# Optimization experiments

Measured on AMD Instinct MI355X. Metric: run time of the kernel, lower is better.

Reference implementation:

```python
import jax, jax.numpy as jnp
import numpy as np

KS = 3          # deformable kernel size
N = KS * KS     # 9 sampling points
PAD = 1         # zero padding before sampling


def setup_inputs() -> dict:
    key = jax.random.key(0)
    k = jax.random.split(key, 4)
    b, c, h, w = 8, 64, 128, 128
    x = jax.random.normal(k[0], (b, c, h, w), jnp.float32)
    # offset-prediction conv: Conv2d(c, 2*N, 3, padding=1, stride=1) with bias
    w_off = jax.random.normal(k[1], (2 * N, c, 3, 3), jnp.float32) * 0.01
    b_off = jax.random.normal(k[2], (2 * N,), jnp.float32) * 0.01
    # main conv: Conv2d(c, c, 3, stride=3, bias=None) applied to rearranged samples
    w_conv = jax.random.normal(k[3], (c, c, KS, KS), jnp.float32) * (1.0 / np.sqrt(c * N))
    return {"x": x, "w_off": w_off, "b_off": b_off, "w_conv": w_conv}


def _deform_conv2d(x, w_off, b_off, w_conv):
    b, c, h, w = x.shape
    # 1) predict offsets: (b, 2N, h, w)
    offset = jax.lax.conv_general_dilated(
        x, w_off, (1, 1), ((PAD, PAD), (PAD, PAD)),
        dimension_numbers=("NCHW", "OIHW", "NCHW"))
    offset = offset + b_off[None, :, None, None]
    offset = offset.transpose(0, 2, 3, 1)  # (b, h, w, 2N), first N = rows, last N = cols

    # 2) sampling positions p = p_0 + p_n + offset (in zero-padded coords)
    dx, dy = jnp.meshgrid(
        jnp.arange(-(KS - 1) // 2, (KS - 1) // 2 + 1),
        jnp.arange(-(KS - 1) // 2, (KS - 1) // 2 + 1), indexing="ij")
    pn_x = dx.reshape(-1).astype(x.dtype)  # (N,)
    pn_y = dy.reshape(-1).astype(x.dtype)
    r0 = jnp.arange(1, h + 1, dtype=x.dtype)  # p_0 starts at 1 (padding shift)
    c0 = jnp.arange(1, w + 1, dtype=x.dtype)
    p_x = offset[..., :N] + pn_x + r0[None, :, None, None]   # (b,h,w,N)
    p_y = offset[..., N:] + pn_y + c0[None, None, :, None]

    xp = jnp.pad(x, ((0, 0), (0, 0), (PAD, PAD), (PAD, PAD)))
    Hp, Wp = h + 2 * PAD, w + 2 * PAD

    fx = jnp.floor(p_x)
    fy = jnp.floor(p_y)
    q_lt_x = jnp.clip(fx, 0, Hp - 1).astype(jnp.int32)
    q_lt_y = jnp.clip(fy, 0, Wp - 1).astype(jnp.int32)
    q_rb_x = jnp.clip(fx + 1, 0, Hp - 1).astype(jnp.int32)
    q_rb_y = jnp.clip(fy + 1, 0, Wp - 1).astype(jnp.int32)
    p_x = jnp.clip(p_x, 0, Hp - 1)
    p_y = jnp.clip(p_y, 0, Wp - 1)

    # bilinear weights (b,h,w,N); q values are non-differentiable (int)
    g_lt = (1 + (q_lt_x - p_x)) * (1 + (q_lt_y - p_y))
    g_rb = (1 - (q_rb_x - p_x)) * (1 - (q_rb_y - p_y))
    g_lb = (1 + (q_lt_x - p_x)) * (1 - (q_rb_y - p_y))
    g_rt = (1 - (q_rb_x - p_x)) * (1 + (q_lt_y - p_y))

    xp_flat = xp.reshape(b, c, Hp * Wp)

    def gather(qx, qy):
        idx = (qx * Wp + qy).reshape(b, 1, h * w * N)
        out = jnp.take_along_axis(
            xp_flat, jnp.broadcast_to(idx, (b, c, h * w * N)), axis=2)
        return out.reshape(b, c, h, w, N)

    x_off = (g_lt[:, None] * gather(q_lt_x, q_lt_y)
             + g_rb[:, None] * gather(q_rb_x, q_rb_y)
             + g_lb[:, None] * gather(q_lt_x, q_rb_y)
             + g_rt[:, None] * gather(q_rb_x, q_lt_y))  # (b,c,h,w,N)

    # 3) final KSxKS conv with stride KS over the rearranged samples is exactly
    #    a contraction over the N sampling points (sample n = kernel tap (i,j), n=i*KS+j)
    out = jnp.einsum("bchwn,ocn->bohw", x_off, w_conv.reshape(c, c, N))
    return out


def reference(x, w_off, b_off, w_conv):
    return _deform_conv2d(x, w_off, b_off, w_conv) + x
```

## Files before the change

kernel.cpp:

```cpp
#include <hip/hip_runtime.h>


typedef _Float16 h2    __attribute__((ext_vector_type(2)));
typedef _Float16 f16x8 __attribute__((ext_vector_type(8)));
typedef float    f32x4 __attribute__((ext_vector_type(4)));

#define MFMAH(a, b, c) __builtin_amdgcn_mfma_f32_16x16x32_f16(a, b, c, 0, 0, 0)

__device__ __forceinline__ unsigned short f2h(float f) {
    return __builtin_bit_cast(unsigned short, (_Float16)f);
}
__device__ __forceinline__ float h2f_bits(unsigned u) {
    return (float)__builtin_bit_cast(_Float16, (unsigned short)(u & 0xffffu));
}
__device__ __forceinline__ unsigned dup16(float g) {
    _Float16 t = (_Float16)g;
    h2 r = {t, t};
    return __builtin_bit_cast(unsigned, r);
}

__global__ __launch_bounds__(256) void k_prep_xt(const float* __restrict__ x,
                                                 unsigned short* __restrict__ xt) {
    __shared__ float xs[64][129];
    const int bh = blockIdx.x;
    const int h = bh & 127, b = bh >> 7;
    const float* xr = x + ((size_t)b * 64 * 128 + h) * 128;
    for (int idx = threadIdx.x; idx < 8192; idx += 256) {
        int c = idx >> 7, w = idx & 127;
        xs[c][w] = xr[(size_t)c * 16384 + w];
    }
    __syncthreads();
    unsigned short* xto = xt + ((size_t)bh << 13);
    for (int j = threadIdx.x; j < 1024; j += 256) {
        int w = j >> 3, c0 = (j & 7) << 3;
        unsigned short tmp[8];
#pragma unroll
        for (int e = 0; e < 8; ++e) tmp[e] = f2h(xs[c0 + e][w]);
        *(uint4*)(xto + w * 64 + c0) = *(const uint4*)tmp;
    }
}

__global__ void k_prep_w(const float* __restrict__ w_conv, const float* __restrict__ w_off,
                         unsigned short* __restrict__ w_m2, unsigned short* __restrict__ woff2) {
    int t = blockIdx.x * 256 + threadIdx.x;
    if (t < 36864) {
        int r = t & 511;
        int fid = t >> 9;
        int l15 = r >> 5, q4 = (r >> 3) & 3, e = t & 7;
        int chunk = fid & 1, of = (fid >> 1) & 3, n = fid >> 3;
        int o = of * 16 + l15, c = chunk * 32 + q4 * 8 + e;
        w_m2[t] = f2h(w_conv[(o * 64 + c) * 9 + n]);
    }
    int t2 = t - 36864;
    if (t2 >= 0 && t2 < 18432) {
        int r = t2 & 511;
        int fid = t2 >> 9;
        int l15 = r >> 5, q4 = (r >> 3) & 3, e = t2 & 7;
        int kc = fid & 1, half = (fid >> 1) & 1, rj = fid >> 2;
        int k = half * 16 + l15, c = kc * 32 + q4 * 8 + e;
        woff2[t2] = (k < 18) ? f2h(w_off[(k * 64 + c) * 9 + rj]) : (unsigned short)0;
    }
}

__global__ __launch_bounds__(256, 4) void k_fused(
    const float* __restrict__ x, const unsigned short* __restrict__ xt,
    const unsigned short* __restrict__ w_m2, const unsigned short* __restrict__ woff2,
    const float* __restrict__ b_off, float* __restrict__ out) {

    __shared__ __align__(16) unsigned char raw[4 * 70 * 128];
    __shared__ __align__(16) _Float16 offv[64 * 24];
    __shared__ int sfb;

    const int wk = ((blockIdx.x & 7) << 8) + (blockIdx.x >> 3);
    const int b = wk >> 8, h = (wk >> 1) & 127, wt = (wk & 1) << 6;

    const int tid  = threadIdx.x;
    const int lane = tid & 63, wid = tid >> 6;
    const int l15  = lane & 15, q4 = lane >> 4;
    const int lofs = ((l15 << 2) + q4) << 3;
    const int px   = wid * 16 + l15;

    const unsigned short* xtb = xt + ((size_t)b << 20);
    const _Float16* wmh  = (const _Float16*)w_m2;

    if (tid == 0) sfb = 0;

    for (int idx = tid; idx < 2240; idx += 256) {
        int rec = idx >> 3, cc = idx & 7;
        int rl = rec / 70, col = rec - rl * 70;
        int xr = h - 2 + rl, xc = wt - 3 + col;
        uint4 v = make_uint4(0, 0, 0, 0);
        if (xr >= 0 && xr < 128 && xc >= 0 && xc < 128)
            v = *(const uint4*)(xtb + ((((size_t)xr << 7) + xc) << 6) + (cc << 3));
        *(uint4*)(raw + (rec << 7) + ((cc ^ (col & 7)) << 4)) = v;
    }
    __syncthreads();

    {
        f32x4 o0 = {0.f, 0.f, 0.f, 0.f}, o1 = {0.f, 0.f, 0.f, 0.f};
#pragma unroll
        for (int rj = 0; rj < 9; ++rj) {
            const int dr = rj / 3, dj = rj % 3;
            const int colw = px + dj + 2;
            const int recb = (dr + 1) * 70 + colw;
            const int swz  = colw & 7;
#pragma unroll
            for (int kc = 0; kc < 2; ++kc) {
                f16x8 bfrag = *(const f16x8*)(raw + (recb << 7) + ((((kc << 2) + q4) ^ swz) << 4));
                f16x8 a0 = *(const f16x8*)((const _Float16*)woff2 + ((((rj * 2 + 0) << 1) + kc) << 9) + lofs);
                f16x8 a1 = *(const f16x8*)((const _Float16*)woff2 + ((((rj * 2 + 1) << 1) + kc) << 9) + lofs);
                o0 = MFMAH(a0, bfrag, o0);
                o1 = MFMAH(a1, bfrag, o1);
            }
        }
        float4 bo = *(const float4*)(b_off + (q4 << 2));
        float2 bo2 = *(const float2*)(b_off + 16);
        const float bov[4] = {bo.x, bo.y, bo.z, bo.w};
#pragma unroll
        for (int rg = 0; rg < 4; ++rg) {
            int o = (q4 << 2) + rg;
            offv[px * 24 + o] = (_Float16)(o0[rg] + bov[rg]);
            if (q4 == 0 && rg < 2) offv[px * 24 + 16 + rg] = (_Float16)(o1[rg] + (rg ? bo2.y : bo2.x));
        }
    }
    __syncthreads();

    for (int idx = tid; idx < 576; idx += 256) {
        const int n = idx >> 6, p = idx & 63;
        const int dr = n / 3, dj = n % 3;
        float ox = (float)offv[p * 24 + n], oy = (float)offv[p * 24 + 9 + n];
        float pxf = (float)(h + dr) + ox, pyf = (float)(wt + p + dj) + oy;
        float fx = floorf(pxf), fy = floorf(pyf);
        int qx0 = (int)fminf(fmaxf(fx, 0.f), 129.f);
        int qx1 = (int)fminf(fmaxf(fx + 1.f, 0.f), 129.f);
        int qy0 = (int)fminf(fmaxf(fy, 0.f), 129.f);
        int qy1 = (int)fminf(fmaxf(fy + 1.f, 0.f), 129.f);
        int r0 = qx0 - h - dr, r1 = qx1 - h - dr;
        int c0 = qy0 - wt + 2, c1 = qy1 - wt + 2;
        bool oow = (r0 < -1) | (r0 > 2) | (r1 < -1) | (r1 > 2) |
                   (c0 < 0) | (c0 >= 70) | (c1 < 0) | (c1 >= 70);
        if (oow) sfb = 1;
    }
    __syncthreads();
    const bool slow = (sfb != 0);

    f32x4 acc[4];
#pragma unroll
    for (int of = 0; of < 4; ++of) acc[of] = (f32x4){0.f, 0.f, 0.f, 0.f};

    auto blend = [&](const uint4* clo, const uint4* chi, uint4 gq, f16x8& bfr0, f16x8& bfr1) {
        h2 g0 = __builtin_bit_cast(h2, gq.x), g1 = __builtin_bit_cast(h2, gq.y);
        h2 g2 = __builtin_bit_cast(h2, gq.z), g3 = __builtin_bit_cast(h2, gq.w);
        const unsigned* c0 = (const unsigned*)&clo[0];
        const unsigned* c1 = (const unsigned*)&clo[1];
        const unsigned* c2 = (const unsigned*)&clo[2];
        const unsigned* c3 = (const unsigned*)&clo[3];
        const unsigned* e0 = (const unsigned*)&chi[0];
        const unsigned* e1 = (const unsigned*)&chi[1];
        const unsigned* e2 = (const unsigned*)&chi[2];
        const unsigned* e3 = (const unsigned*)&chi[3];
        unsigned owl[4], owh[4];
#pragma unroll
        for (int d = 0; d < 4; ++d) {
            h2 sl = __builtin_bit_cast(h2, c0[d]) * g0;
            sl = __builtin_elementwise_fma(__builtin_bit_cast(h2, c1[d]), g1, sl);
            sl = __builtin_elementwise_fma(__builtin_bit_cast(h2, c2[d]), g2, sl);
            sl = __builtin_elementwise_fma(__builtin_bit_cast(h2, c3[d]), g3, sl);
            owl[d] = __builtin_bit_cast(unsigned, sl);
            h2 sh = __builtin_bit_cast(h2, e0[d]) * g0;
            sh = __builtin_elementwise_fma(__builtin_bit_cast(h2, e1[d]), g1, sh);
            sh = __builtin_elementwise_fma(__builtin_bit_cast(h2, e2[d]), g2, sh);
            sh = __builtin_elementwise_fma(__builtin_bit_cast(h2, e3[d]), g3, sh);
            owh[d] = __builtin_bit_cast(unsigned, sh);
        }
        bfr0 = __builtin_bit_cast(f16x8, *(const uint4*)owl);
        bfr1 = __builtin_bit_cast(f16x8, *(const uint4*)owh);
    };

    if (!slow) {
        const unsigned* op = (const unsigned*)(offv + px * 24);
        uint4 oA = *(const uint4*)op;
        uint4 oB = *(const uint4*)(op + 4);
        unsigned oC = op[8];
        const unsigned ow[9] = {oA.x, oA.y, oA.z, oA.w, oB.x, oB.y, oB.z, oB.w, oC};
#define OX(n) h2f_bits(ow[(n) >> 1] >> (((n) & 1) << 4))
#define OY(n) h2f_bits(ow[(9 + (n)) >> 1] >> (((9 + (n)) & 1) << 4))

        uint4 pf[3];
        int pcol[3], pcc[3];
#pragma unroll
        for (int k = 0; k < 3; ++k) {
            int idx = tid + (k << 8);
            bool v = idx < 560;
            int rec = idx >> 3;
            pcol[k] = v ? rec : 0;
            pcc[k]  = idx & 7;
            int xr = h + 2, xc = wt - 3 + pcol[k];
            uint4 vv = make_uint4(0, 0, 0, 0);
            if (v && xr < 128 && xc >= 0 && xc < 128)
                vv = *(const uint4*)(xtb + ((((size_t)xr << 7) + xc) << 6) + (pcc[k] << 3));
            if (!v) pcol[k] = -1;
            pf[k] = vv;
        }

#define TAP(n)                                                                           \
        {                                                                                \
            constexpr int dr = (n) / 3, dj = (n) % 3;                                    \
            const _Float16* wn = wmh + ((n) << 12);                                      \
            f16x8 wa0[4], wa1[4];                                                        \
            _Pragma("unroll")                                                            \
            for (int of = 0; of < 4; ++of) {                                             \
                wa0[of] = *(const f16x8*)(wn + (((of << 1) + 0) << 9) + lofs);           \
                wa1[of] = *(const f16x8*)(wn + (((of << 1) + 1) << 9) + lofs);           \
            }                                                                            \
            float ox = OX(n), oy = OY(n);                                                \
            float pxf = (float)(h + dr) + ox, pyf = (float)(wt + px + dj) + oy;          \
            float fx = floorf(pxf), fy = floorf(pyf);                                    \
            float qx0f = fminf(fmaxf(fx, 0.f), 129.f);                                   \
            float qx1f = fminf(fmaxf(fx + 1.f, 0.f), 129.f);                             \
            float qy0f = fminf(fmaxf(fy, 0.f), 129.f);                                   \
            float qy1f = fminf(fmaxf(fy + 1.f, 0.f), 129.f);                             \
            float pxc = fminf(fmaxf(pxf, 0.f), 129.f);                                   \
            float pyc = fminf(fmaxf(pyf, 0.f), 129.f);                                   \
            float ax0 = 1.f + (qx0f - pxc), ax1 = 1.f - (qx1f - pxc);                    \
            float ay0 = 1.f + (qy0f - pyc), ay1 = 1.f - (qy1f - pyc);                    \
            int s0 = ((((int)qx0f + 1 - h) & 3) * 70) << 7;                              \
            int s1 = ((((int)qx1f + 1 - h) & 3) * 70) << 7;                              \
            int c0 = (int)qy0f - wt + 2, c1 = (int)qy1f - wt + 2;                        \
            int blt = s0 + (c0 << 7), brb = s1 + (c1 << 7);                              \
            int blb = s0 + (c1 << 7), brt = s1 + (c0 << 7);                              \
            int z0 = ((q4 ^ c0) & 7) << 4, z1 = ((q4 ^ c1) & 7) << 4;                    \
            uint4 clo[4], chi[4];                                                        \
            clo[0] = *(const uint4*)(raw + blt + z0); chi[0] = *(const uint4*)(raw + blt + (z0 ^ 64)); \
            clo[1] = *(const uint4*)(raw + brb + z1); chi[1] = *(const uint4*)(raw + brb + (z1 ^ 64)); \
            clo[2] = *(const uint4*)(raw + blb + z1); chi[2] = *(const uint4*)(raw + blb + (z1 ^ 64)); \
            clo[3] = *(const uint4*)(raw + brt + z0); chi[3] = *(const uint4*)(raw + brt + (z0 ^ 64)); \
            uint4 gq = make_uint4(dup16(ax0 * ay0), dup16(ax1 * ay1),                    \
                                  dup16(ax0 * ay1), dup16(ax1 * ay0));                   \
            f16x8 bfr0, bfr1;                                                            \
            blend(clo, chi, gq, bfr0, bfr1);                                             \
            _Pragma("unroll")                                                            \
            for (int of = 0; of < 4; ++of) {                                             \
                acc[of] = MFMAH(wa0[of], bfr0, acc[of]);                                 \
                acc[of] = MFMAH(wa1[of], bfr1, acc[of]);                                 \
            }                                                                            \
        }

        TAP(0) TAP(1) TAP(2)
        __syncthreads();
#pragma unroll
        for (int k = 0; k < 3; ++k)
            if (pcol[k] >= 0)
                *(uint4*)(raw + ((0 * 70 + pcol[k]) << 7) + ((pcc[k] ^ (pcol[k] & 7)) << 4)) = pf[k];
        __syncthreads();
#pragma unroll
        for (int k = 0; k < 3; ++k) {
            int idx = tid + (k << 8);
            bool v = idx < 560;
            int rec = idx >> 3;
            pcol[k] = v ? rec : -1;
            pcc[k]  = idx & 7;
            int xr = h + 3, xc = wt - 3 + rec;
            uint4 vv = make_uint4(0, 0, 0, 0);
            if (v && xr < 128 && xc >= 0 && xc < 128)
                vv = *(const uint4*)(xtb + ((((size_t)xr << 7) + xc) << 6) + (pcc[k] << 3));
            pf[k] = vv;
        }
        TAP(3) TAP(4) TAP(5)
        __syncthreads();
#pragma unroll
        for (int k = 0; k < 3; ++k)
            if (pcol[k] >= 0)
                *(uint4*)(raw + ((1 * 70 + pcol[k]) << 7) + ((pcc[k] ^ (pcol[k] & 7)) << 4)) = pf[k];
        __syncthreads();
        TAP(6) TAP(7) TAP(8)
#undef TAP
#undef OX
#undef OY
    } else {
        for (int n = 0; n < 9; ++n) {
            const int dr = n / 3, dj = n % 3;
            float ox = (float)offv[px * 24 + n], oy = (float)offv[px * 24 + 9 + n];
            float pxf = (float)(h + dr) + ox, pyf = (float)(wt + px + dj) + oy;
            float fx = floorf(pxf), fy = floorf(pyf);
            float qx0f = fminf(fmaxf(fx, 0.f), 129.f);
            float qx1f = fminf(fmaxf(fx + 1.f, 0.f), 129.f);
            float qy0f = fminf(fmaxf(fy, 0.f), 129.f);
            float qy1f = fminf(fmaxf(fy + 1.f, 0.f), 129.f);
            float pxc = fminf(fmaxf(pxf, 0.f), 129.f);
            float pyc = fminf(fmaxf(pyf, 0.f), 129.f);
            float ax0 = 1.f + (qx0f - pxc), ax1 = 1.f - (qx1f - pxc);
            float ay0 = 1.f + (qy0f - pyc), ay1 = 1.f - (qy1f - pyc);
            int qx[2] = {(int)qx0f, (int)qx1f};
            int qy[2] = {(int)qy0f, (int)qy1f};
            uint4 clo[4], chi[4];
            const int rsel[4] = {0, 1, 0, 1}, csel[4] = {0, 1, 1, 0};
#pragma unroll
            for (int j = 0; j < 4; ++j) {
                int rx = qx[rsel[j]], ry = qy[csel[j]];
                bool v = (rx >= 1) & (rx <= 128) & (ry >= 1) & (ry <= 128);
                clo[j] = make_uint4(0, 0, 0, 0);
                chi[j] = make_uint4(0, 0, 0, 0);
                if (v) {
                    const unsigned short* gp = xtb + ((((size_t)(rx - 1) << 7) + (ry - 1)) << 6);
                    clo[j] = *(const uint4*)(gp + (q4 << 3));
                    chi[j] = *(const uint4*)(gp + (q4 << 3) + 32);
                }
            }
            uint4 gq = make_uint4(dup16(ax0 * ay0), dup16(ax1 * ay1),
                                  dup16(ax0 * ay1), dup16(ax1 * ay0));
            f16x8 bfr0, bfr1;
            blend(clo, chi, gq, bfr0, bfr1);
            const _Float16* wn = wmh + (n << 12);
#pragma unroll
            for (int of = 0; of < 4; ++of) {
                f16x8 a0 = *(const f16x8*)(wn + (((of << 1) + 0) << 9) + lofs);
                f16x8 a1 = *(const f16x8*)(wn + (((of << 1) + 1) << 9) + lofs);
                acc[of] = MFMAH(a0, bfr0, acc[of]);
                acc[of] = MFMAH(a1, bfr1, acc[of]);
            }
        }
    }

    const size_t obase = ((size_t)b * 64 * 128 + h) * 128 + wt + px;
#pragma unroll
    for (int of = 0; of < 4; ++of)
#pragma unroll
        for (int rg = 0; rg < 4; ++rg) {
            size_t a = obase + (size_t)((of << 4) + (q4 << 2) + rg) * 16384;
            out[a] = acc[of][rg] + x[a];
        }
}

extern "C" void kernel_launch(void* const* d_in, const int* in_sizes, int n_in,
                              void* d_out, int out_size, void* d_ws, size_t ws_size,
                              hipStream_t stream) {
    const float* x      = (const float*)d_in[0];
    const float* w_off  = (const float*)d_in[1];
    const float* b_off  = (const float*)d_in[2];
    const float* w_conv = (const float*)d_in[3];

    unsigned short* xt    = (unsigned short*)d_ws;
    unsigned short* w_m2  = xt + (size_t)8 * 128 * 128 * 64;
    unsigned short* woff2 = w_m2 + 9 * 64 * 64;

    hipLaunchKernelGGL(k_prep_xt, dim3(1024), dim3(256), 0, stream, x, xt);
    hipLaunchKernelGGL(k_prep_w,  dim3(216),  dim3(256), 0, stream, w_conv, w_off, w_m2, woff2);
    hipLaunchKernelGGL(k_fused,   dim3(2048), dim3(256), 0, stream,
                       x, xt, w_m2, woff2, b_off, (float*)d_out);
}
```

Before: 84.55 us.

## Process two output rows per block to reuse weights and halo rows

Each fused block now computes two adjacent output rows instead of one, halving the grid. The shared halo grows from 4 to 5 rows, so the overlapping input rows are loaded once and shared by both rows. The main-conv weight fragments for each tap are loaded once and used for both rows' MFMAs. In exchange the kernel holds twice the accumulators and a larger LDS footprint, and its launch bounds drop from 4 to 3 waves, which lowers occupancy and may cause register pressure.

```diff
diff --git a/kernel.cpp b/kernel.cpp
--- a/kernel.cpp
+++ b/kernel.cpp
@@ -62,17 +62,17 @@
     }
 }
 
-__global__ __launch_bounds__(256, 4) void k_fused(
+__global__ __launch_bounds__(256, 3) void k_fused(
     const float* __restrict__ x, const unsigned short* __restrict__ xt,
     const unsigned short* __restrict__ w_m2, const unsigned short* __restrict__ woff2,
     const float* __restrict__ b_off, float* __restrict__ out) {
 
-    __shared__ __align__(16) unsigned char raw[4 * 70 * 128];
-    __shared__ __align__(16) _Float16 offv[64 * 24];
+    __shared__ __align__(16) unsigned char raw[5 * 70 * 128];
+    __shared__ __align__(16) _Float16 offv[2][64][24];
     __shared__ int sfb;
 
-    const int wk = ((blockIdx.x & 7) << 8) + (blockIdx.x >> 3);
-    const int b = wk >> 8, h = (wk >> 1) & 127, wt = (wk & 1) << 6;
+    const int wk = ((blockIdx.x & 7) << 7) | (blockIdx.x >> 3);
+    const int b = wk >> 7, h = ((wk >> 1) & 63) << 1, wt = (wk & 1) << 6;
 
     const int tid  = threadIdx.x;
     const int lane = tid & 63, wid = tid >> 6;
@@ -85,7 +85,7 @@
 
     if (tid == 0) sfb = 0;
 
-    for (int idx = tid; idx < 2240; idx += 256) {
+    for (int idx = tid; idx < 2800; idx += 256) {
         int rec = idx >> 3, cc = idx & 7;
         int rl = rec / 70, col = rec - rl * 70;
         int xr = h - 2 + rl, xc = wt - 3 + col;
@@ -96,13 +96,14 @@
     }
     __syncthreads();
 
-    {
+#pragma unroll
+    for (int rr = 0; rr < 2; ++rr) {
         f32x4 o0 = {0.f, 0.f, 0.f, 0.f}, o1 = {0.f, 0.f, 0.f, 0.f};
 #pragma unroll
         for (int rj = 0; rj < 9; ++rj) {
             const int dr = rj / 3, dj = rj % 3;
             const int colw = px + dj + 2;
-            const int recb = (dr + 1) * 70 + colw;
+            const int recb = (rr + dr + 1) * 70 + colw;
             const int swz  = colw & 7;
 #pragma unroll
             for (int kc = 0; kc < 2; ++kc) {
@@ -119,34 +120,40 @@
 #pragma unroll
         for (int rg = 0; rg < 4; ++rg) {
             int o = (q4 << 2) + rg;
-            offv[px * 24 + o] = (_Float16)(o0[rg] + bov[rg]);
-            if (q4 == 0 && rg < 2) offv[px * 24 + 16 + rg] = (_Float16)(o1[rg] + (rg ? bo2.y : bo2.x));
+            offv[rr][px][o] = (_Float16)(o0[rg] + bov[rg]);
+            if (q4 == 0 && rg < 2) offv[rr][px][16 + rg] = (_Float16)(o1[rg] + (rg ? bo2.y : bo2.x));
         }
     }
     __syncthreads();
 
-    for (int idx = tid; idx < 576; idx += 256) {
-        const int n = idx >> 6, p = idx & 63;
-        const int dr = n / 3, dj = n % 3;
-        float ox = (float)offv[p * 24 + n], oy = (float)offv[p * 24 + 9 + n];
-        float pxf = (float)(h + dr) + ox, pyf = (float)(wt + p + dj) + oy;
+    for (int idx = tid; idx < 1152; idx += 256) {
+        const int p = idx & 63;
+        int rest = idx >> 6;
+        const int rr = (rest >= 9) ? 1 : 0;
+        const int n = rest - rr * 9;
+        const int g = n / 3, dj = n % 3;
+        float ox = (float)offv[rr][p][n], oy = (float)offv[rr][p][9 + n];
+        float pxf = (float)(h + rr + g) + ox, pyf = (float)(wt + p + dj) + oy;
         float fx = floorf(pxf), fy = floorf(pyf);
         int qx0 = (int)fminf(fmaxf(fx, 0.f), 129.f);
         int qx1 = (int)fminf(fmaxf(fx + 1.f, 0.f), 129.f);
         int qy0 = (int)fminf(fmaxf(fy, 0.f), 129.f);
         int qy1 = (int)fminf(fmaxf(fy + 1.f, 0.f), 129.f);
-        int r0 = qx0 - h - dr, r1 = qx1 - h - dr;
+        int t0 = qx0 + 1 - h - g, t1 = qx1 + 1 - h - g;
         int c0 = qy0 - wt + 2, c1 = qy1 - wt + 2;
-        bool oow = (r0 < -1) | (r0 > 2) | (r1 < -1) | (r1 > 2) |
-                   (c0 < 0) | (c0 >= 70) | (c1 < 0) | (c1 >= 70);
+        bool oow = ((unsigned)t0 > 4u) | ((unsigned)t1 > 4u) |
+                   ((unsigned)c0 > 69u) | ((unsigned)c1 > 69u);
         if (oow) sfb = 1;
     }
     __syncthreads();
     const bool slow = (sfb != 0);
 
-    f32x4 acc[4];
-#pragma unroll
-    for (int of = 0; of < 4; ++of) acc[of] = (f32x4){0.f, 0.f, 0.f, 0.f};
+    f32x4 acc0[4], acc1[4];
+#pragma unroll
+    for (int of = 0; of < 4; ++of) {
+        acc0[of] = (f32x4){0.f, 0.f, 0.f, 0.f};
+        acc1[of] = (f32x4){0.f, 0.f, 0.f, 0.f};
+    }
 
     auto blend = [&](const uint4* clo, const uint4* chi, uint4 gq, f16x8& bfr0, f16x8& bfr1) {
         h2 g0 = __builtin_bit_cast(h2, gq.x), g1 = __builtin_bit_cast(h2, gq.y);
@@ -178,13 +185,16 @@
     };
 
     if (!slow) {
-        const unsigned* op = (const unsigned*)(offv + px * 24);
-        uint4 oA = *(const uint4*)op;
-        uint4 oB = *(const uint4*)(op + 4);
-        unsigned oC = op[8];
-        const unsigned ow[9] = {oA.x, oA.y, oA.z, oA.w, oB.x, oB.y, oB.z, oB.w, oC};
-#define OX(n) h2f_bits(ow[(n) >> 1] >> (((n) & 1) << 4))
-#define OY(n) h2f_bits(ow[(9 + (n)) >> 1] >> (((9 + (n)) & 1) << 4))
+        const unsigned* op0 = (const unsigned*)&offv[0][px][0];
+        const unsigned* op1 = (const unsigned*)&offv[1][px][0];
+        uint4 oA0 = *(const uint4*)op0, oB0 = *(const uint4*)(op0 + 4);
+        unsigned oC0 = op0[8];
+        uint4 oA1 = *(const uint4*)op1, oB1 = *(const uint4*)(op1 + 4);
+        unsigned oC1 = op1[8];
+        const unsigned ow0[9] = {oA0.x, oA0.y, oA0.z, oA0.w, oB0.x, oB0.y, oB0.z, oB0.w, oC0};
+        const unsigned ow1[9] = {oA1.x, oA1.y, oA1.z, oA1.w, oB1.x, oB1.y, oB1.z, oB1.w, oC1};
+#define OXQ(arr, n) h2f_bits(arr[(n) >> 1] >> (((n) & 1) << 4))
+#define OYQ(arr, n) h2f_bits(arr[(9 + (n)) >> 1] >> (((9 + (n)) & 1) << 4))
 
         uint4 pf[3];
         int pcol[3], pcc[3];
@@ -193,28 +203,20 @@
             int idx = tid + (k << 8);
             bool v = idx < 560;
             int rec = idx >> 3;
-            pcol[k] = v ? rec : 0;
-            pcc[k]  = idx & 7;
-            int xr = h + 2, xc = wt - 3 + pcol[k];
+            pcc[k] = idx & 7;
+            int xr = h + 3, xc = wt - 3 + rec;
             uint4 vv = make_uint4(0, 0, 0, 0);
             if (v && xr < 128 && xc >= 0 && xc < 128)
                 vv = *(const uint4*)(xtb + ((((size_t)xr << 7) + xc) << 6) + (pcc[k] << 3));
-            if (!v) pcol[k] = -1;
+            pcol[k] = v ? rec : -1;
             pf[k] = vv;
         }
 
-#define TAP(n)                                                                           \
+#define TAPR(n, OWA, ACC)                                                                \
         {                                                                                \
-            constexpr int dr = (n) / 3, dj = (n) % 3;                                    \
-            const _Float16* wn = wmh + ((n) << 12);                                      \
-            f16x8 wa0[4], wa1[4];                                                        \
-            _Pragma("unroll")                                                            \
-            for (int of = 0; of < 4; ++of) {                                             \
-                wa0[of] = *(const f16x8*)(wn + (((of << 1) + 0) << 9) + lofs);           \
-                wa1[of] = *(const f16x8*)(wn + (((of << 1) + 1) << 9) + lofs);           \
-            }                                                                            \
-            float ox = OX(n), oy = OY(n);                                                \
-            float pxf = (float)(h + dr) + ox, pyf = (float)(wt + px + dj) + oy;          \
+            constexpr int g = (n) / 3, dj = (n) % 3;                                     \
+            float ox = OXQ(OWA, n), oy = OYQ(OWA, n);                                    \
+            float pxf = rowbase + (float)g + ox, pyf = (float)(wt + px + dj) + oy;       \
             float fx = floorf(pxf), fy = floorf(pyf);                                    \
             float qx0f = fminf(fmaxf(fx, 0.f), 129.f);                                   \
             float qx1f = fminf(fmaxf(fx + 1.f, 0.f), 129.f);                             \
@@ -224,11 +226,12 @@
             float pyc = fminf(fmaxf(pyf, 0.f), 129.f);                                   \
             float ax0 = 1.f + (qx0f - pxc), ax1 = 1.f - (qx1f - pxc);                    \
             float ay0 = 1.f + (qy0f - pyc), ay1 = 1.f - (qy1f - pyc);                    \
-            int s0 = ((((int)qx0f + 1 - h) & 3) * 70) << 7;                              \
-            int s1 = ((((int)qx1f + 1 - h) & 3) * 70) << 7;                              \
+            int u0 = (int)qx0f + 1 - h, u1 = (int)qx1f + 1 - h;                          \
+            int s0 = (u0 - (u0 >= 5 ? 5 : 0)) * 70;                                      \
+            int s1 = (u1 - (u1 >= 5 ? 5 : 0)) * 70;                                      \
             int c0 = (int)qy0f - wt + 2, c1 = (int)qy1f - wt + 2;                        \
-            int blt = s0 + (c0 << 7), brb = s1 + (c1 << 7);                              \
-            int blb = s0 + (c1 << 7), brt = s1 + (c0 << 7);                              \
+            int blt = (s0 + c0) << 7, brb = (s1 + c1) << 7;                              \
+            int blb = (s0 + c1) << 7, brt = (s1 + c0) << 7;                              \
             int z0 = ((q4 ^ c0) & 7) << 4, z1 = ((q4 ^ c1) & 7) << 4;                    \
             uint4 clo[4], chi[4];                                                        \
             clo[0] = *(const uint4*)(raw + blt + z0); chi[0] = *(const uint4*)(raw + blt + (z0 ^ 64)); \
@@ -241,9 +244,22 @@
             blend(clo, chi, gq, bfr0, bfr1);                                             \
             _Pragma("unroll")                                                            \
             for (int of = 0; of < 4; ++of) {                                             \
-                acc[of] = MFMAH(wa0[of], bfr0, acc[of]);                                 \
-                acc[of] = MFMAH(wa1[of], bfr1, acc[of]);                                 \
+                ACC[of] = MFMAH(wa0[of], bfr0, ACC[of]);                                 \
+                ACC[of] = MFMAH(wa1[of], bfr1, ACC[of]);                                 \
             }                                                                            \
+        }
+
+#define TAP(n)                                                                           \
+        {                                                                                \
+            const _Float16* wn = wmh + ((n) << 12);                                      \
+            f16x8 wa0[4], wa1[4];                                                        \
+            _Pragma("unroll")                                                            \
+            for (int of = 0; of < 4; ++of) {                                             \
+                wa0[of] = *(const f16x8*)(wn + (((of << 1) + 0) << 9) + lofs);           \
+                wa1[of] = *(const f16x8*)(wn + (((of << 1) + 1) << 9) + lofs);           \
+            }                                                                            \
+            { const float rowbase = (float)h;       TAPR(n, ow0, acc0) }                 \
+            { const float rowbase = (float)(h + 1); TAPR(n, ow1, acc1) }                 \
         }
 
         TAP(0) TAP(1) TAP(2)
@@ -258,12 +274,12 @@
             int idx = tid + (k << 8);
             bool v = idx < 560;
             int rec = idx >> 3;
-            pcol[k] = v ? rec : -1;
-            pcc[k]  = idx & 7;
-            int xr = h + 3, xc = wt - 3 + rec;
+            pcc[k] = idx & 7;
+            int xr = h + 4, xc = wt - 3 + rec;
             uint4 vv = make_uint4(0, 0, 0, 0);
             if (v && xr < 128 && xc >= 0 && xc < 128)
                 vv = *(const uint4*)(xtb + ((((size_t)xr << 7) + xc) << 6) + (pcc[k] << 3));
+            pcol[k] = v ? rec : -1;
             pf[k] = vv;
         }
         TAP(3) TAP(4) TAP(5)
@@ -275,50 +291,54 @@
         __syncthreads();
         TAP(6) TAP(7) TAP(8)
 #undef TAP
-#undef OX
-#undef OY
+#undef TAPR
+#undef OXQ
+#undef OYQ
     } else {
-        for (int n = 0; n < 9; ++n) {
-            const int dr = n / 3, dj = n % 3;
-            float ox = (float)offv[px * 24 + n], oy = (float)offv[px * 24 + 9 + n];
-            float pxf = (float)(h + dr) + ox, pyf = (float)(wt + px + dj) + oy;
-            float fx = floorf(pxf), fy = floorf(pyf);
-            float qx0f = fminf(fmaxf(fx, 0.f), 129.f);
-            float qx1f = fminf(fmaxf(fx + 1.f, 0.f), 129.f);
-            float qy0f = fminf(fmaxf(fy, 0.f), 129.f);
-            float qy1f = fminf(fmaxf(fy + 1.f, 0.f), 129.f);
-            float pxc = fminf(fmaxf(pxf, 0.f), 129.f);
-            float pyc = fminf(fmaxf(pyf, 0.f), 129.f);
-            float ax0 = 1.f + (qx0f - pxc), ax1 = 1.f - (qx1f - pxc);
-            float ay0 = 1.f + (qy0f - pyc), ay1 = 1.f - (qy1f - pyc);
-            int qx[2] = {(int)qx0f, (int)qx1f};
-            int qy[2] = {(int)qy0f, (int)qy1f};
-            uint4 clo[4], chi[4];
-            const int rsel[4] = {0, 1, 0, 1}, csel[4] = {0, 1, 1, 0};
-#pragma unroll
-            for (int j = 0; j < 4; ++j) {
-                int rx = qx[rsel[j]], ry = qy[csel[j]];
-                bool v = (rx >= 1) & (rx <= 128) & (ry >= 1) & (ry <= 128);
-                clo[j] = make_uint4(0, 0, 0, 0);
-                chi[j] = make_uint4(0, 0, 0, 0);
-                if (v) {
-                    const unsigned short* gp = xtb + ((((size_t)(rx - 1) << 7) + (ry - 1)) << 6);
-                    clo[j] = *(const uint4*)(gp + (q4 << 3));
-                    chi[j] = *(const uint4*)(gp + (q4 << 3) + 32);
+        for (int rr = 0; rr < 2; ++rr) {
+            f32x4* ACC = rr ? acc1 : acc0;
+            for (int n = 0; n < 9; ++n) {
+                const int g = n / 3, dj = n % 3;
+                float ox = (float)offv[rr][px][n], oy = (float)offv[rr][px][9 + n];
+                float pxf = (float)(h + rr + g) + ox, pyf = (float)(wt + px + dj) + oy;
+                float fx = floorf(pxf), fy = floorf(pyf);
+                float qx0f = fminf(fmaxf(fx, 0.f), 129.f);
+                float qx1f = fminf(fmaxf(fx + 1.f, 0.f), 129.f);
+                float qy0f = fminf(fmaxf(fy, 0.f), 129.f);
+                float qy1f = fminf(fmaxf(fy + 1.f, 0.f), 129.f);
+                float pxc = fminf(fmaxf(pxf, 0.f), 129.f);
+                float pyc = fminf(fmaxf(pyf, 0.f), 129.f);
+                float ax0 = 1.f + (qx0f - pxc), ax1 = 1.f - (qx1f - pxc);
+                float ay0 = 1.f + (qy0f - pyc), ay1 = 1.f - (qy1f - pyc);
+                int qx[2] = {(int)qx0f, (int)qx1f};
+                int qy[2] = {(int)qy0f, (int)qy1f};
+                uint4 clo[4], chi[4];
+                const int rsel[4] = {0, 1, 0, 1}, csel[4] = {0, 1, 1, 0};
+#pragma unroll
+                for (int j = 0; j < 4; ++j) {
+                    int rx = qx[rsel[j]], ry = qy[csel[j]];
+                    bool v = (rx >= 1) & (rx <= 128) & (ry >= 1) & (ry <= 128);
+                    clo[j] = make_uint4(0, 0, 0, 0);
+                    chi[j] = make_uint4(0, 0, 0, 0);
+                    if (v) {
+                        const unsigned short* gp = xtb + ((((size_t)(rx - 1) << 7) + (ry - 1)) << 6);
+                        clo[j] = *(const uint4*)(gp + (q4 << 3));
+                        chi[j] = *(const uint4*)(gp + (q4 << 3) + 32);
+                    }
+                }
+                uint4 gq = make_uint4(dup16(ax0 * ay0), dup16(ax1 * ay1),
+                                      dup16(ax0 * ay1), dup16(ax1 * ay0));
+                f16x8 bfr0, bfr1;
+                blend(clo, chi, gq, bfr0, bfr1);
+                const _Float16* wn = wmh + (n << 12);
+#pragma unroll
+                for (int of = 0; of < 4; ++of) {
+                    f16x8 a0 = *(const f16x8*)(wn + (((of << 1) + 0) << 9) + lofs);
+                    f16x8 a1 = *(const f16x8*)(wn + (((of << 1) + 1) << 9) + lofs);
+                    ACC[of] = MFMAH(a0, bfr0, ACC[of]);
+                    ACC[of] = MFMAH(a1, bfr1, ACC[of]);
                 }
             }
-            uint4 gq = make_uint4(dup16(ax0 * ay0), dup16(ax1 * ay1),
-                                  dup16(ax0 * ay1), dup16(ax1 * ay0));
-            f16x8 bfr0, bfr1;
-            blend(clo, chi, gq, bfr0, bfr1);
-            const _Float16* wn = wmh + (n << 12);
-#pragma unroll
-            for (int of = 0; of < 4; ++of) {
-                f16x8 a0 = *(const f16x8*)(wn + (((of << 1) + 0) << 9) + lofs);
-                f16x8 a1 = *(const f16x8*)(wn + (((of << 1) + 1) << 9) + lofs);
-                acc[of] = MFMAH(a0, bfr0, acc[of]);
-                acc[of] = MFMAH(a1, bfr1, acc[of]);
-            }
         }
     }
 
@@ -328,7 +348,8 @@
 #pragma unroll
         for (int rg = 0; rg < 4; ++rg) {
             size_t a = obase + (size_t)((of << 4) + (q4 << 2) + rg) * 16384;
-            out[a] = acc[of][rg] + x[a];
+            out[a] = acc0[of][rg] + x[a];
+            out[a + 128] = acc1[of][rg] + x[a + 128];
         }
 }
 
@@ -346,6 +367,6 @@
 
     hipLaunchKernelGGL(k_prep_xt, dim3(1024), dim3(256), 0, stream, x, xt);
     hipLaunchKernelGGL(k_prep_w,  dim3(216),  dim3(256), 0, stream, w_conv, w_off, w_m2, woff2);
-    hipLaunchKernelGGL(k_fused,   dim3(2048), dim3(256), 0, stream,
+    hipLaunchKernelGGL(k_fused,   dim3(1024), dim3(256), 0, stream,
                        x, xt, w_m2, woff2, b_off, (float*)d_out);
 }
```

Measured after the change: 110.4 us. +30.6%, slower.

## Stage all six input rows in LDS and software-pipeline tap loads with MFMA

Applied to the files above, without the earlier changes.

Loads all six needed xt rows into shared memory up front instead of streaming two rows in with extra barriers mid-loop, which removes four __syncthreads and the rolling prefetch. The offset conv and the nine-tap sampling loop are double-buffered so the next step's LDS and weight loads are issued while the current MFMAs run, with split accumulators in the offset conv. The residual x loads are hoisted before the main loop. In exchange, LDS use grows and the occupancy hint drops from 4 to 2 blocks per SM, with higher register pressure.

```diff
diff --git a/kernel.cpp b/kernel.cpp
--- a/kernel.cpp
+++ b/kernel.cpp
@@ -17,6 +17,36 @@
     _Float16 t = (_Float16)g;
     h2 r = {t, t};
     return __builtin_bit_cast(unsigned, r);
+}
+
+__device__ __forceinline__ void blend8(const uint4* clo, const uint4* chi, uint4 gq,
+                                       f16x8& bfr0, f16x8& bfr1) {
+    h2 g0 = __builtin_bit_cast(h2, gq.x), g1 = __builtin_bit_cast(h2, gq.y);
+    h2 g2 = __builtin_bit_cast(h2, gq.z), g3 = __builtin_bit_cast(h2, gq.w);
+    const unsigned* c0 = (const unsigned*)&clo[0];
+    const unsigned* c1 = (const unsigned*)&clo[1];
+    const unsigned* c2 = (const unsigned*)&clo[2];
+    const unsigned* c3 = (const unsigned*)&clo[3];
+    const unsigned* e0 = (const unsigned*)&chi[0];
+    const unsigned* e1 = (const unsigned*)&chi[1];
+    const unsigned* e2 = (const unsigned*)&chi[2];
+    const unsigned* e3 = (const unsigned*)&chi[3];
+    unsigned owl[4], owh[4];
+#pragma unroll
+    for (int d = 0; d < 4; ++d) {
+        h2 sl = __builtin_bit_cast(h2, c0[d]) * g0;
+        sl = __builtin_elementwise_fma(__builtin_bit_cast(h2, c1[d]), g1, sl);
+        sl = __builtin_elementwise_fma(__builtin_bit_cast(h2, c2[d]), g2, sl);
+        sl = __builtin_elementwise_fma(__builtin_bit_cast(h2, c3[d]), g3, sl);
+        owl[d] = __builtin_bit_cast(unsigned, sl);
+        h2 sh = __builtin_bit_cast(h2, e0[d]) * g0;
+        sh = __builtin_elementwise_fma(__builtin_bit_cast(h2, e1[d]), g1, sh);
+        sh = __builtin_elementwise_fma(__builtin_bit_cast(h2, e2[d]), g2, sh);
+        sh = __builtin_elementwise_fma(__builtin_bit_cast(h2, e3[d]), g3, sh);
+        owh[d] = __builtin_bit_cast(unsigned, sh);
+    }
+    bfr0 = __builtin_bit_cast(f16x8, *(const uint4*)owl);
+    bfr1 = __builtin_bit_cast(f16x8, *(const uint4*)owh);
 }
 
 __global__ __launch_bounds__(256) void k_prep_xt(const float* __restrict__ x,
@@ -62,12 +92,12 @@
     }
 }
 
-__global__ __launch_bounds__(256, 4) void k_fused(
+__global__ __launch_bounds__(256, 2) void k_fused(
     const float* __restrict__ x, const unsigned short* __restrict__ xt,
     const unsigned short* __restrict__ w_m2, const unsigned short* __restrict__ woff2,
     const float* __restrict__ b_off, float* __restrict__ out) {
 
-    __shared__ __align__(16) unsigned char raw[4 * 70 * 128];
+    __shared__ __align__(16) unsigned char raw[6 * 70 * 128];
     __shared__ __align__(16) _Float16 offv[64 * 24];
     __shared__ int sfb;
 
@@ -82,10 +112,11 @@
 
     const unsigned short* xtb = xt + ((size_t)b << 20);
     const _Float16* wmh  = (const _Float16*)w_m2;
+    const _Float16* wofh = (const _Float16*)woff2;
 
     if (tid == 0) sfb = 0;
 
-    for (int idx = tid; idx < 2240; idx += 256) {
+    for (int idx = tid; idx < 3360; idx += 256) {
         int rec = idx >> 3, cc = idx & 7;
         int rl = rec / 70, col = rec - rl * 70;
         int xr = h - 2 + rl, xc = wt - 3 + col;
@@ -97,22 +128,47 @@
     __syncthreads();
 
     {
-        f32x4 o0 = {0.f, 0.f, 0.f, 0.f}, o1 = {0.f, 0.f, 0.f, 0.f};
-#pragma unroll
-        for (int rj = 0; rj < 9; ++rj) {
-            const int dr = rj / 3, dj = rj % 3;
-            const int colw = px + dj + 2;
-            const int recb = (dr + 1) * 70 + colw;
-            const int swz  = colw & 7;
-#pragma unroll
-            for (int kc = 0; kc < 2; ++kc) {
-                f16x8 bfrag = *(const f16x8*)(raw + (recb << 7) + ((((kc << 2) + q4) ^ swz) << 4));
-                f16x8 a0 = *(const f16x8*)((const _Float16*)woff2 + ((((rj * 2 + 0) << 1) + kc) << 9) + lofs);
-                f16x8 a1 = *(const f16x8*)((const _Float16*)woff2 + ((((rj * 2 + 1) << 1) + kc) << 9) + lofs);
-                o0 = MFMAH(a0, bfrag, o0);
-                o1 = MFMAH(a1, bfrag, o1);
-            }
-        }
+        f32x4 o0a = {0,0,0,0}, o0b = {0,0,0,0}, o1a = {0,0,0,0}, o1b = {0,0,0,0};
+        f16x8 bfgA, af0A, af1A, bfgB, af0B, af1B;
+
+#define ALOAD(s, S)                                                                      \
+        {                                                                                \
+            constexpr int rj = (s) >> 1, kc = (s) & 1;                                   \
+            const int colw = px + (rj % 3) + 2;                                          \
+            const int recb = ((rj / 3) + 1) * 70 + colw;                                 \
+            bfg##S = *(const f16x8*)(raw + (recb << 7) + ((((kc << 2) + q4) ^ (colw & 7)) << 4)); \
+            af0##S = *(const f16x8*)(wofh + ((((rj * 2 + 0) << 1) + kc) << 9) + lofs);   \
+            af1##S = *(const f16x8*)(wofh + ((((rj * 2 + 1) << 1) + kc) << 9) + lofs);   \
+        }
+#define AEXEC(S, P)                                                                      \
+        {                                                                                \
+            o0##P = MFMAH(af0##S, bfg##S, o0##P);                                        \
+            o1##P = MFMAH(af1##S, bfg##S, o1##P);                                        \
+        }
+        ALOAD(0, A)
+        ALOAD(1, B)  AEXEC(A, a)
+        ALOAD(2, A)  AEXEC(B, b)
+        ALOAD(3, B)  AEXEC(A, a)
+        ALOAD(4, A)  AEXEC(B, b)
+        ALOAD(5, B)  AEXEC(A, a)
+        ALOAD(6, A)  AEXEC(B, b)
+        ALOAD(7, B)  AEXEC(A, a)
+        ALOAD(8, A)  AEXEC(B, b)
+        ALOAD(9, B)  AEXEC(A, a)
+        ALOAD(10, A) AEXEC(B, b)
+        ALOAD(11, B) AEXEC(A, a)
+        ALOAD(12, A) AEXEC(B, b)
+        ALOAD(13, B) AEXEC(A, a)
+        ALOAD(14, A) AEXEC(B, b)
+        ALOAD(15, B) AEXEC(A, a)
+        ALOAD(16, A) AEXEC(B, b)
+        ALOAD(17, B) AEXEC(A, a)
+                     AEXEC(B, b)
+#undef ALOAD
+#undef AEXEC
+        f32x4 o0, o1;
+#pragma unroll
+        for (int rg = 0; rg < 4; ++rg) { o0[rg] = o0a[rg] + o0b[rg]; o1[rg] = o1a[rg] + o1b[rg]; }
         float4 bo = *(const float4*)(b_off + (q4 << 2));
         float2 bo2 = *(const float2*)(b_off + 16);
         const float bov[4] = {bo.x, bo.y, bo.z, bo.w};
@@ -127,94 +183,51 @@
 
     for (int idx = tid; idx < 576; idx += 256) {
         const int n = idx >> 6, p = idx & 63;
-        const int dr = n / 3, dj = n % 3;
+        const int g = n / 3, dj = n % 3;
         float ox = (float)offv[p * 24 + n], oy = (float)offv[p * 24 + 9 + n];
-        float pxf = (float)(h + dr) + ox, pyf = (float)(wt + p + dj) + oy;
+        float pxf = (float)(h + g) + ox, pyf = (float)(wt + p + dj) + oy;
         float fx = floorf(pxf), fy = floorf(pyf);
-        int qx0 = (int)fminf(fmaxf(fx, 0.f), 129.f);
-        int qx1 = (int)fminf(fmaxf(fx + 1.f, 0.f), 129.f);
-        int qy0 = (int)fminf(fmaxf(fy, 0.f), 129.f);
-        int qy1 = (int)fminf(fmaxf(fy + 1.f, 0.f), 129.f);
-        int r0 = qx0 - h - dr, r1 = qx1 - h - dr;
-        int c0 = qy0 - wt + 2, c1 = qy1 - wt + 2;
-        bool oow = (r0 < -1) | (r0 > 2) | (r1 < -1) | (r1 > 2) |
-                   (c0 < 0) | (c0 >= 70) | (c1 < 0) | (c1 >= 70);
+        int wr0 = (int)fminf(fmaxf(fx, 0.f), 129.f) + 1 - h;
+        int wr1 = (int)fminf(fmaxf(fx + 1.f, 0.f), 129.f) + 1 - h;
+        int c0 = (int)fminf(fmaxf(fy, 0.f), 129.f) - wt + 2;
+        int c1 = (int)fminf(fmaxf(fy + 1.f, 0.f), 129.f) - wt + 2;
+        bool oow = ((unsigned)wr0 > 5u) | ((unsigned)wr1 > 5u) |
+                   ((unsigned)c0 > 69u) | ((unsigned)c1 > 69u);
         if (oow) sfb = 1;
     }
     __syncthreads();
     const bool slow = (sfb != 0);
 
+    const size_t obase = ((size_t)b * 64 * 128 + h) * 128 + wt + px;
+    float xres[4][4];
+#pragma unroll
+    for (int of = 0; of < 4; ++of)
+#pragma unroll
+        for (int rg = 0; rg < 4; ++rg)
+            xres[of][rg] = x[obase + (size_t)((of << 4) + (q4 << 2) + rg) * 16384];
+
     f32x4 acc[4];
 #pragma unroll
     for (int of = 0; of < 4; ++of) acc[of] = (f32x4){0.f, 0.f, 0.f, 0.f};
-
-    auto blend = [&](const uint4* clo, const uint4* chi, uint4 gq, f16x8& bfr0, f16x8& bfr1) {
-        h2 g0 = __builtin_bit_cast(h2, gq.x), g1 = __builtin_bit_cast(h2, gq.y);
-        h2 g2 = __builtin_bit_cast(h2, gq.z), g3 = __builtin_bit_cast(h2, gq.w);
-        const unsigned* c0 = (const unsigned*)&clo[0];
-        const unsigned* c1 = (const unsigned*)&clo[1];
-        const unsigned* c2 = (const unsigned*)&clo[2];
-        const unsigned* c3 = (const unsigned*)&clo[3];
-        const unsigned* e0 = (const unsigned*)&chi[0];
-        const unsigned* e1 = (const unsigned*)&chi[1];
-        const unsigned* e2 = (const unsigned*)&chi[2];
-        const unsigned* e3 = (const unsigned*)&chi[3];
-        unsigned owl[4], owh[4];
-#pragma unroll
-        for (int d = 0; d < 4; ++d) {
-            h2 sl = __builtin_bit_cast(h2, c0[d]) * g0;
-            sl = __builtin_elementwise_fma(__builtin_bit_cast(h2, c1[d]), g1, sl);
-            sl = __builtin_elementwise_fma(__builtin_bit_cast(h2, c2[d]), g2, sl);
-            sl = __builtin_elementwise_fma(__builtin_bit_cast(h2, c3[d]), g3, sl);
-            owl[d] = __builtin_bit_cast(unsigned, sl);
-            h2 sh = __builtin_bit_cast(h2, e0[d]) * g0;
-            sh = __builtin_elementwise_fma(__builtin_bit_cast(h2, e1[d]), g1, sh);
-            sh = __builtin_elementwise_fma(__builtin_bit_cast(h2, e2[d]), g2, sh);
-            sh = __builtin_elementwise_fma(__builtin_bit_cast(h2, e3[d]), g3, sh);
-            owh[d] = __builtin_bit_cast(unsigned, sh);
-        }
-        bfr0 = __builtin_bit_cast(f16x8, *(const uint4*)owl);
-        bfr1 = __builtin_bit_cast(f16x8, *(const uint4*)owh);
-    };
 
     if (!slow) {
         const unsigned* op = (const unsigned*)(offv + px * 24);
         uint4 oA = *(const uint4*)op;
         uint4 oB = *(const uint4*)(op + 4);
         unsigned oC = op[8];
-        const unsigned ow[9] = {oA.x, oA.y, oA.z, oA.w, oB.x, oB.y, oB.z, oB.w, oC};
-#define OX(n) h2f_bits(ow[(n) >> 1] >> (((n) & 1) << 4))
-#define OY(n) h2f_bits(ow[(9 + (n)) >> 1] >> (((9 + (n)) & 1) << 4))
-
-        uint4 pf[3];
-        int pcol[3], pcc[3];
-#pragma unroll
-        for (int k = 0; k < 3; ++k) {
-            int idx = tid + (k << 8);
-            bool v = idx < 560;
-            int rec = idx >> 3;
-            pcol[k] = v ? rec : 0;
-            pcc[k]  = idx & 7;
-            int xr = h + 2, xc = wt - 3 + pcol[k];
-            uint4 vv = make_uint4(0, 0, 0, 0);
-            if (v && xr < 128 && xc >= 0 && xc < 128)
-                vv = *(const uint4*)(xtb + ((((size_t)xr << 7) + xc) << 6) + (pcc[k] << 3));
-            if (!v) pcol[k] = -1;
-            pf[k] = vv;
-        }
-
-#define TAP(n)                                                                           \
+        const unsigned owr[9] = {oA.x, oA.y, oA.z, oA.w, oB.x, oB.y, oB.z, oB.w, oC};
+#define OXQ(n) h2f_bits(owr[(n) >> 1] >> (((n) & 1) << 4))
+#define OYQ(n) h2f_bits(owr[(9 + (n)) >> 1] >> (((9 + (n)) & 1) << 4))
+
+        uint4 cloA[4], chiA[4], cloB[4], chiB[4];
+        uint4 gqA, gqB;
+        f16x8 waA[8], waB[8];
+
+#define TAPLOAD(n, S)                                                                    \
         {                                                                                \
-            constexpr int dr = (n) / 3, dj = (n) % 3;                                    \
-            const _Float16* wn = wmh + ((n) << 12);                                      \
-            f16x8 wa0[4], wa1[4];                                                        \
-            _Pragma("unroll")                                                            \
-            for (int of = 0; of < 4; ++of) {                                             \
-                wa0[of] = *(const f16x8*)(wn + (((of << 1) + 0) << 9) + lofs);           \
-                wa1[of] = *(const f16x8*)(wn + (((of << 1) + 1) << 9) + lofs);           \
-            }                                                                            \
-            float ox = OX(n), oy = OY(n);                                                \
-            float pxf = (float)(h + dr) + ox, pyf = (float)(wt + px + dj) + oy;          \
+            constexpr int g = (n) / 3, dj = (n) % 3;                                     \
+            float ox = OXQ(n), oy = OYQ(n);                                              \
+            float pxf = (float)(h + g) + ox, pyf = (float)(wt + px + dj) + oy;           \
             float fx = floorf(pxf), fy = floorf(pyf);                                    \
             float qx0f = fminf(fmaxf(fx, 0.f), 129.f);                                   \
             float qx1f = fminf(fmaxf(fx + 1.f, 0.f), 129.f);                             \
@@ -224,64 +237,59 @@
             float pyc = fminf(fmaxf(pyf, 0.f), 129.f);                                   \
             float ax0 = 1.f + (qx0f - pxc), ax1 = 1.f - (qx1f - pxc);                    \
             float ay0 = 1.f + (qy0f - pyc), ay1 = 1.f - (qy1f - pyc);                    \
-            int s0 = ((((int)qx0f + 1 - h) & 3) * 70) << 7;                              \
-            int s1 = ((((int)qx1f + 1 - h) & 3) * 70) << 7;                              \
+            int r0 = ((int)qx0f + 1 - h) * 70, r1 = ((int)qx1f + 1 - h) * 70;            \
             int c0 = (int)qy0f - wt + 2, c1 = (int)qy1f - wt + 2;                        \
-            int blt = s0 + (c0 << 7), brb = s1 + (c1 << 7);                              \
-            int blb = s0 + (c1 << 7), brt = s1 + (c0 << 7);                              \
+            int blt = (r0 + c0) << 7, brb = (r1 + c1) << 7;                              \
+            int blb = (r0 + c1) << 7, brt = (r1 + c0) << 7;                              \
             int z0 = ((q4 ^ c0) & 7) << 4, z1 = ((q4 ^ c1) & 7) << 4;                    \
-            uint4 clo[4], chi[4];                                                        \
-            clo[0] = *(const uint4*)(raw + blt + z0); chi[0] = *(const uint4*)(raw + blt + (z0 ^ 64)); \
-            clo[1] = *(const uint4*)(raw + brb + z1); chi[1] = *(const uint4*)(raw + brb + (z1 ^ 64)); \
-            clo[2] = *(const uint4*)(raw + blb + z1); chi[2] = *(const uint4*)(raw + blb + (z1 ^ 64)); \
-            clo[3] = *(const uint4*)(raw + brt + z0); chi[3] = *(const uint4*)(raw + brt + (z0 ^ 64)); \
-            uint4 gq = make_uint4(dup16(ax0 * ay0), dup16(ax1 * ay1),                    \
-                                  dup16(ax0 * ay1), dup16(ax1 * ay0));                   \
-            f16x8 bfr0, bfr1;                                                            \
-            blend(clo, chi, gq, bfr0, bfr1);                                             \
+            clo##S[0] = *(const uint4*)(raw + blt + z0);                                 \
+            chi##S[0] = *(const uint4*)(raw + blt + (z0 ^ 64));                          \
+            clo##S[1] = *(const uint4*)(raw + brb + z1);                                 \
+            chi##S[1] = *(const uint4*)(raw + brb + (z1 ^ 64));                          \
+            clo##S[2] = *(const uint4*)(raw + blb + z1);                                 \
+            chi##S[2] = *(const uint4*)(raw + blb + (z1 ^ 64));                          \
+            chi##S[3] = *(const uint4*)(raw + brt + (z0 ^ 64));                          \
+            clo##S[3] = *(const uint4*)(raw + brt + z0);                                 \
+            gq##S = make_uint4(dup16(ax0 * ay0), dup16(ax1 * ay1),                       \
+                               dup16(ax0 * ay1), dup16(ax1 * ay0));                      \
+            const _Float16* wn = wmh + ((n) << 12);                                      \
             _Pragma("unroll")                                                            \
             for (int of = 0; of < 4; ++of) {                                             \
-                acc[of] = MFMAH(wa0[of], bfr0, acc[of]);                                 \
-                acc[of] = MFMAH(wa1[of], bfr1, acc[of]);                                 \
+                wa##S[2 * of]     = *(const f16x8*)(wn + (((of << 1) + 0) << 9) + lofs); \
+                wa##S[2 * of + 1] = *(const f16x8*)(wn + (((of << 1) + 1) << 9) + lofs); \
             }                                                                            \
         }
 
-        TAP(0) TAP(1) TAP(2)
-        __syncthreads();
-#pragma unroll
-        for (int k = 0; k < 3; ++k)
-            if (pcol[k] >= 0)
-                *(uint4*)(raw + ((0 * 70 + pcol[k]) << 7) + ((pcc[k] ^ (pcol[k] & 7)) << 4)) = pf[k];
-        __syncthreads();
-#pragma unroll
-        for (int k = 0; k < 3; ++k) {
-            int idx = tid + (k << 8);
-            bool v = idx < 560;
-            int rec = idx >> 3;
-            pcol[k] = v ? rec : -1;
-            pcc[k]  = idx & 7;
-            int xr = h + 3, xc = wt - 3 + rec;
-            uint4 vv = make_uint4(0, 0, 0, 0);
-            if (v && xr < 128 && xc >= 0 && xc < 128)
-                vv = *(const uint4*)(xtb + ((((size_t)xr << 7) + xc) << 6) + (pcc[k] << 3));
-            pf[k] = vv;
-        }
-        TAP(3) TAP(4) TAP(5)
-        __syncthreads();
-#pragma unroll
-        for (int k = 0; k < 3; ++k)
-            if (pcol[k] >= 0)
-                *(uint4*)(raw + ((1 * 70 + pcol[k]) << 7) + ((pcc[k] ^ (pcol[k] & 7)) << 4)) = pf[k];
-        __syncthreads();
-        TAP(6) TAP(7) TAP(8)
-#undef TAP
-#undef OX
-#undef OY
+#define TAPEXEC(S)                                                                       \
+        {                                                                                \
+            f16x8 bfr0, bfr1;                                                            \
+            blend8(clo##S, chi##S, gq##S, bfr0, bfr1);                                   \
+            _Pragma("unroll")                                                            \
+            for (int of = 0; of < 4; ++of) {                                             \
+                acc[of] = MFMAH(wa##S[2 * of],     bfr0, acc[of]);                       \
+                acc[of] = MFMAH(wa##S[2 * of + 1], bfr1, acc[of]);                       \
+            }                                                                            \
+        }
+
+        TAPLOAD(0, A)
+        TAPLOAD(1, B) TAPEXEC(A)
+        TAPLOAD(2, A) TAPEXEC(B)
+        TAPLOAD(3, B) TAPEXEC(A)
+        TAPLOAD(4, A) TAPEXEC(B)
+        TAPLOAD(5, B) TAPEXEC(A)
+        TAPLOAD(6, A) TAPEXEC(B)
+        TAPLOAD(7, B) TAPEXEC(A)
+        TAPLOAD(8, A) TAPEXEC(B)
+                      TAPEXEC(A)
+#undef TAPLOAD
+#undef TAPEXEC
+#undef OXQ
+#undef OYQ
     } else {
         for (int n = 0; n < 9; ++n) {
-            const int dr = n / 3, dj = n % 3;
+            const int g = n / 3, dj = n % 3;
             float ox = (float)offv[px * 24 + n], oy = (float)offv[px * 24 + 9 + n];
-            float pxf = (float)(h + dr) + ox, pyf = (float)(wt + px + dj) + oy;
+            float pxf = (float)(h + g) + ox, pyf = (float)(wt + px + dj) + oy;
             float fx = floorf(pxf), fy = floorf(pyf);
             float qx0f = fminf(fmaxf(fx, 0.f), 129.f);
             float qx1f = fminf(fmaxf(fx + 1.f, 0.f), 129.f);
@@ -310,7 +318,7 @@
             uint4 gq = make_uint4(dup16(ax0 * ay0), dup16(ax1 * ay1),
                                   dup16(ax0 * ay1), dup16(ax1 * ay0));
             f16x8 bfr0, bfr1;
-            blend(clo, chi, gq, bfr0, bfr1);
+            blend8(clo, chi, gq, bfr0, bfr1);
             const _Float16* wn = wmh + (n << 12);
 #pragma unroll
             for (int of = 0; of < 4; ++of) {
@@ -322,14 +330,11 @@
         }
     }
 
-    const size_t obase = ((size_t)b * 64 * 128 + h) * 128 + wt + px;
 #pragma unroll
     for (int of = 0; of < 4; ++of)
 #pragma unroll
-        for (int rg = 0; rg < 4; ++rg) {
-            size_t a = obase + (size_t)((of << 4) + (q4 << 2) + rg) * 16384;
-            out[a] = acc[of][rg] + x[a];
-        }
+        for (int rg = 0; rg < 4; ++rg)
+            out[obase + (size_t)((of << 4) + (q4 << 2) + rg) * 16384] = acc[of][rg] + xres[of][rg];
 }
 
 extern "C" void kernel_launch(void* const* d_in, const int* in_sizes, int n_in,
```

New measurement: 91.60 us. 8.3% more time.
